# Kernel optimization log

Hardware: AMD Instinct MI355X
Metric: run time of the kernel (lower is better)

The kernel has to match this reference:

```python
import jax, jax.numpy as jnp
import numpy as np

TEMPERATURE = 0.5


def setup_inputs() -> dict:
    key = jax.random.key(0)
    k1, k2 = jax.random.split(key)
    B, D = 4096, 256
    return {
        "features": jax.random.normal(k1, (B, D), dtype=jnp.float32),
        "transformed_features": jax.random.normal(k2, (B, D), dtype=jnp.float32),
    }


def reference(features, transformed_features):
    B = features.shape[0]
    N = 2 * B
    all_features = jnp.concatenate([features, transformed_features], axis=0)  # [2B, D]
    # F.normalize(dim=-1): L2 normalize with eps clamp of 1e-12 on the norm
    norm = jnp.maximum(jnp.linalg.norm(all_features, axis=-1, keepdims=True), 1e-12)
    all_features = all_features / norm
    sim = jnp.matmul(all_features, all_features.T)  # [2B, 2B]
    # positive pairs: diag at offsets +B and -B
    pos = jnp.concatenate([jnp.diagonal(sim, offset=B), jnp.diagonal(sim, offset=-B)], axis=0)  # [2B]
    numerator = jnp.exp(pos / TEMPERATURE)
    # torch code multiplies sim by (1 - eye) BEFORE exp, so diagonal contributes exp(0)=1 to the sum
    sim_no_diag = sim * (1.0 - jnp.eye(N, dtype=sim.dtype))
    denominator = jnp.exp(sim_no_diag / TEMPERATURE).sum(axis=1)  # [2B]
    losses = -jnp.log(numerator / denominator)
    return jnp.sum(losses) / N
```

## Files before the change

### kernel.cpp

```cpp
#include <hip/hip_runtime.h>

#define B_ROWS 4096
#define N_ROWS 8192
#define DDIM   256
#define IT2    2.885390081777927f

#define BM 128
#define BN 128
#define BK 64
#define SPLITS 32
#define CT_PER_BLOCK (N_ROWS / BN / SPLITS)
#define NPARTS (SPLITS * 2)

typedef unsigned short ushort_t;
typedef __bf16 bf16x8 __attribute__((ext_vector_type(8)));
typedef float  f32x4  __attribute__((ext_vector_type(4)));

__device__ __forceinline__ ushort_t f2bf(float x) {
    union { float f; unsigned u; } a; a.f = x;
    unsigned r = a.u + 0x7fffu + ((a.u >> 16) & 1u);
    return (ushort_t)(r >> 16);
}

__device__ __forceinline__ void gload_lds16(const void* g, void* l) {
    __builtin_amdgcn_global_load_lds(
        (const __attribute__((address_space(1))) unsigned int*)g,
        (__attribute__((address_space(3))) unsigned int*)l,
        16, 0, 0);
}

__global__ __launch_bounds__(256) void k_normalize(
        const float* __restrict__ feats, const float* __restrict__ tfeats,
        ushort_t* __restrict__ Xb, float* __restrict__ norms) {
    int w = threadIdx.x >> 6, l = threadIdx.x & 63;
    int row = blockIdx.x * 4 + w;
    const float* src = (row < B_ROWS) ? feats + (size_t)row * DDIM
                                      : tfeats + (size_t)(row - B_ROWS) * DDIM;
    float4 v = ((const float4*)src)[l];
    float ss = v.x*v.x + v.y*v.y + v.z*v.z + v.w*v.w;
    #pragma unroll
    for (int m = 1; m < 64; m <<= 1) ss += __shfl_xor(ss, m);
    float nrm = fmaxf(sqrtf(ss), 1e-12f);
    float inv = 1.0f / nrm;
    ushort4 o;
    o.x = f2bf(v.x * inv); o.y = f2bf(v.y * inv);
    o.z = f2bf(v.z * inv); o.w = f2bf(v.w * inv);
    ((ushort4*)(Xb + (size_t)row * DDIM))[l] = o;
    if (l == 0) norms[row] = nrm;
}

__global__ __launch_bounds__(256) void k_pos(
        const float* __restrict__ feats, const float* __restrict__ tfeats,
        const float* __restrict__ norms, float* __restrict__ posv) {
    int w = threadIdx.x >> 6, l = threadIdx.x & 63;
    int i = blockIdx.x * 4 + w;
    float4 a = ((const float4*)(feats  + (size_t)i * DDIM))[l];
    float4 b = ((const float4*)(tfeats + (size_t)i * DDIM))[l];
    float d = a.x*b.x + a.y*b.y + a.z*b.z + a.w*b.w;
    #pragma unroll
    for (int m = 1; m < 64; m <<= 1) d += __shfl_xor(d, m);
    if (l == 0) posv[i] = d / (norms[i] * norms[i + B_ROWS]);
}

__global__ __launch_bounds__(256) void k_gemm(
        const ushort_t* __restrict__ Xb, float* __restrict__ parts) {
    __shared__ ushort_t ldsA[BM * BK];
    __shared__ ushort_t ldsB[BN * BK];

    int bid = blockIdx.x;
    int rt = bid >> 5;
    int split = bid & 31;
    int rowbase = rt * BM;
    int t = threadIdx.x;
    int l = t & 63;
    int w = t >> 6;
    int wm = w >> 1, wn = w & 1;

    float sums[4][4];
    #pragma unroll
    for (int m = 0; m < 4; m++)
        #pragma unroll
        for (int j = 0; j < 4; j++) sums[m][j] = 0.0f;

    for (int ct = 0; ct < CT_PER_BLOCK; ++ct) {
        int colbase = (split * CT_PER_BLOCK + ct) * BN;
        f32x4 acc[4][4];
        #pragma unroll
        for (int m = 0; m < 4; m++)
            #pragma unroll
            for (int n = 0; n < 4; n++) acc[m][n] = (f32x4){0.f, 0.f, 0.f, 0.f};

        for (int kb = 0; kb < DDIM; kb += BK) {
            #pragma unroll
            for (int i = 0; i < 4; i++) {
                int o   = (i * 256 + t) * 16;
                int row = o >> 7;
                int cb  = o & 127;
                int scb = cb ^ ((row & 7) << 4);
                const char* ga = (const char*)Xb +
                    ((size_t)(rowbase + row) * DDIM + kb) * 2 + scb;
                gload_lds16(ga, (char*)ldsA + o);
                const char* gb = (const char*)Xb +
                    ((size_t)(colbase + row) * DDIM + kb) * 2 + scb;
                gload_lds16(gb, (char*)ldsB + o);
            }
            __syncthreads();

            #pragma unroll
            for (int ks = 0; ks < 2; ks++) {
                bf16x8 af[4], bfr[4];
                int cbw = ((l >> 4) * 16) + ks * 64;
                #pragma unroll
                for (int m = 0; m < 4; m++) {
                    int row  = wm * 64 + m * 16 + (l & 15);
                    int addr = row * 128 + (cbw ^ ((row & 7) << 4));
                    af[m] = *(const bf16x8*)((const char*)ldsA + addr);
                }
                #pragma unroll
                for (int n = 0; n < 4; n++) {
                    int row  = wn * 64 + n * 16 + (l & 15);
                    int addr = row * 128 + (cbw ^ ((row & 7) << 4));
                    bfr[n] = *(const bf16x8*)((const char*)ldsB + addr);
                }
                #pragma unroll
                for (int m = 0; m < 4; m++)
                    #pragma unroll
                    for (int n = 0; n < 4; n++)
                        acc[m][n] = __builtin_amdgcn_mfma_f32_16x16x32_bf16(
                            af[m], bfr[n], acc[m][n], 0, 0, 0);
            }
            __syncthreads();
        }

        #pragma unroll
        for (int m = 0; m < 4; m++) {
            #pragma unroll
            for (int j = 0; j < 4; j++) {
                int grow = rowbase + wm * 64 + m * 16 + (l >> 4) * 4 + j;
                float s = 0.0f;
                #pragma unroll
                for (int n = 0; n < 4; n++) {
                    int gcol = colbase + wn * 64 + n * 16 + (l & 15);
                    float v = acc[m][n][j];
                    float e = exp2f(v * IT2);
                    s += (grow == gcol) ? 1.0f : e;
                }
                sums[m][j] += s;
            }
        }
    }

    #pragma unroll
    for (int m = 0; m < 4; m++)
        #pragma unroll
        for (int j = 0; j < 4; j++) {
            float v = sums[m][j];
            v += __shfl_xor(v, 1);
            v += __shfl_xor(v, 2);
            v += __shfl_xor(v, 4);
            v += __shfl_xor(v, 8);
            sums[m][j] = v;
        }

    if ((l & 15) == 0) {
        int part = split * 2 + wn;
        #pragma unroll
        for (int m = 0; m < 4; m++)
            #pragma unroll
            for (int j = 0; j < 4; j++) {
                int grow = rowbase + wm * 64 + m * 16 + (l >> 4) * 4 + j;
                parts[(size_t)part * N_ROWS + grow] = sums[m][j];
            }
    }
}

__global__ __launch_bounds__(256) void k_rowreduce(
        const float* __restrict__ parts, float* __restrict__ bsums) {
    int row = blockIdx.x * 256 + threadIdx.x;
    float den = 0.0f;
    #pragma unroll 8
    for (int p = 0; p < NPARTS; p++) den += parts[(size_t)p * N_ROWS + row];
    float v = logf(den);
    #pragma unroll
    for (int m = 1; m < 64; m <<= 1) v += __shfl_xor(v, m);
    __shared__ float red[4];
    if ((threadIdx.x & 63) == 0) red[threadIdx.x >> 6] = v;
    __syncthreads();
    if (threadIdx.x == 0)
        bsums[blockIdx.x] = red[0] + red[1] + red[2] + red[3];
}

__global__ __launch_bounds__(256) void k_final(
        const float* __restrict__ bsums, const float* __restrict__ posv,
        float* __restrict__ out) {
    int t = threadIdx.x;
    float ps = 0.0f;
    for (int i = t; i < B_ROWS; i += 256) ps += posv[i];
    float lg = (t < 32) ? bsums[t] : 0.0f;
    float comb = lg - 4.0f * ps;
    #pragma unroll
    for (int m = 1; m < 64; m <<= 1) comb += __shfl_xor(comb, m);
    __shared__ float red[4];
    if ((t & 63) == 0) red[t >> 6] = comb;
    __syncthreads();
    if (t == 0) out[0] = (red[0] + red[1] + red[2] + red[3]) / (float)N_ROWS;
}

extern "C" void kernel_launch(void* const* d_in, const int* in_sizes, int n_in,
                              void* d_out, int out_size, void* d_ws, size_t ws_size,
                              hipStream_t stream) {
    const float* feats  = (const float*)d_in[0];
    const float* tfeats = (const float*)d_in[1];
    float* out = (float*)d_out;
    char* ws = (char*)d_ws;

    ushort_t* Xb    = (ushort_t*)ws;
    float*    norms = (float*)(ws + 4194304);
    float*    posv  = (float*)(ws + 4227072);
    float*    parts = (float*)(ws + 4243456);
    float*    bsums = (float*)(ws + 6340608);

    k_normalize<<<N_ROWS / 4, 256, 0, stream>>>(feats, tfeats, Xb, norms);
    k_pos      <<<B_ROWS / 4, 256, 0, stream>>>(feats, tfeats, norms, posv);
    k_gemm     <<<64 * SPLITS, 256, 0, stream>>>(Xb, parts);
    k_rowreduce<<<N_ROWS / 256, 256, 0, stream>>>(parts, bsums);
    k_final    <<<1, 256, 0, stream>>>(bsums, posv, out);
}
```

Measured before the change: 119.6 us.

## Exploit symmetry of similarity matrix, compute upper-triangular tiles only, fuse norm and pos

The GEMM now covers only the upper-triangular 128x128 tile pairs (2080 blocks instead of the full grid). Each off-diagonal tile contributes both row sums and column sums of exp(sim/T), which roughly halves the MFMA and exp work. The normalize and positive-pair kernels are merged into one, dropping a launch and a second read of the inputs. In exchange there are twice as many partial buffers to reduce, a serial while-loop to decode each block's tile index, and no multi-tile loop per block to amortize setup.

```diff
diff --git a/kernel.cpp b/kernel.cpp
--- a/kernel.cpp
+++ b/kernel.cpp
@@ -6,11 +6,10 @@
 #define IT2    2.885390081777927f
 
 #define BM 128
-#define BN 128
 #define BK 64
-#define SPLITS 32
-#define CT_PER_BLOCK (N_ROWS / BN / SPLITS)
-#define NPARTS (SPLITS * 2)
+#define NTILE 64
+#define NBLK  2080
+#define NPARTS 128
 
 typedef unsigned short ushort_t;
 typedef __bf16 bf16x8 __attribute__((ext_vector_type(8)));
@@ -29,13 +28,17 @@
         16, 0, 0);
 }
 
-__global__ __launch_bounds__(256) void k_normalize(
+__global__ __launch_bounds__(256) void k_norm_pos(
         const float* __restrict__ feats, const float* __restrict__ tfeats,
-        ushort_t* __restrict__ Xb, float* __restrict__ norms) {
+        ushort_t* __restrict__ Xb, float* __restrict__ posv) {
+    __shared__ float fbuf[2][DDIM];
+    __shared__ float nsh[4];
     int w = threadIdx.x >> 6, l = threadIdx.x & 63;
-    int row = blockIdx.x * 4 + w;
-    const float* src = (row < B_ROWS) ? feats + (size_t)row * DDIM
-                                      : tfeats + (size_t)(row - B_ROWS) * DDIM;
+    int i0 = blockIdx.x * 2;
+    int pair = (w < 2) ? w : (w - 2);
+    int row  = (w < 2) ? (i0 + pair) : (i0 + pair + B_ROWS);
+    const float* src = (w < 2) ? feats + (size_t)(i0 + pair) * DDIM
+                               : tfeats + (size_t)(i0 + pair) * DDIM;
     float4 v = ((const float4*)src)[l];
     float ss = v.x*v.x + v.y*v.y + v.z*v.z + v.w*v.w;
     #pragma unroll
@@ -46,131 +49,135 @@
     o.x = f2bf(v.x * inv); o.y = f2bf(v.y * inv);
     o.z = f2bf(v.z * inv); o.w = f2bf(v.w * inv);
     ((ushort4*)(Xb + (size_t)row * DDIM))[l] = o;
-    if (l == 0) norms[row] = nrm;
-}
-
-__global__ __launch_bounds__(256) void k_pos(
-        const float* __restrict__ feats, const float* __restrict__ tfeats,
-        const float* __restrict__ norms, float* __restrict__ posv) {
-    int w = threadIdx.x >> 6, l = threadIdx.x & 63;
-    int i = blockIdx.x * 4 + w;
-    float4 a = ((const float4*)(feats  + (size_t)i * DDIM))[l];
-    float4 b = ((const float4*)(tfeats + (size_t)i * DDIM))[l];
-    float d = a.x*b.x + a.y*b.y + a.z*b.z + a.w*b.w;
-    #pragma unroll
-    for (int m = 1; m < 64; m <<= 1) d += __shfl_xor(d, m);
-    if (l == 0) posv[i] = d / (norms[i] * norms[i + B_ROWS]);
+    if (w < 2) ((float4*)fbuf[pair])[l] = v;
+    if (l == 0) nsh[w] = nrm;
+    __syncthreads();
+    if (w >= 2) {
+        float4 a = ((const float4*)fbuf[pair])[l];
+        float d = a.x*v.x + a.y*v.y + a.z*v.z + a.w*v.w;
+        #pragma unroll
+        for (int m = 1; m < 64; m <<= 1) d += __shfl_xor(d, m);
+        if (l == 0) posv[i0 + pair] = d / (nsh[pair] * nsh[w]);
+    }
 }
 
 __global__ __launch_bounds__(256) void k_gemm(
         const ushort_t* __restrict__ Xb, float* __restrict__ parts) {
     __shared__ ushort_t ldsA[BM * BK];
-    __shared__ ushort_t ldsB[BN * BK];
-
-    int bid = blockIdx.x;
-    int rt = bid >> 5;
-    int split = bid & 31;
+    __shared__ ushort_t ldsB[BM * BK];
+
+    int idx = blockIdx.x;
+    int rt = 0;
+    while (idx >= (NTILE - rt)) { idx -= (NTILE - rt); rt++; }
+    int ct = rt + idx;
+    bool isdiag = (rt == ct);
+
     int rowbase = rt * BM;
+    int colbase = ct * BM;
     int t = threadIdx.x;
     int l = t & 63;
     int w = t >> 6;
     int wm = w >> 1, wn = w & 1;
 
-    float sums[4][4];
+    f32x4 acc[4][4];
     #pragma unroll
     for (int m = 0; m < 4; m++)
         #pragma unroll
-        for (int j = 0; j < 4; j++) sums[m][j] = 0.0f;
-
-    for (int ct = 0; ct < CT_PER_BLOCK; ++ct) {
-        int colbase = (split * CT_PER_BLOCK + ct) * BN;
-        f32x4 acc[4][4];
-        #pragma unroll
-        for (int m = 0; m < 4; m++)
-            #pragma unroll
-            for (int n = 0; n < 4; n++) acc[m][n] = (f32x4){0.f, 0.f, 0.f, 0.f};
-
-        for (int kb = 0; kb < DDIM; kb += BK) {
-            #pragma unroll
-            for (int i = 0; i < 4; i++) {
-                int o   = (i * 256 + t) * 16;
-                int row = o >> 7;
-                int cb  = o & 127;
-                int scb = cb ^ ((row & 7) << 4);
-                const char* ga = (const char*)Xb +
-                    ((size_t)(rowbase + row) * DDIM + kb) * 2 + scb;
-                gload_lds16(ga, (char*)ldsA + o);
-                const char* gb = (const char*)Xb +
-                    ((size_t)(colbase + row) * DDIM + kb) * 2 + scb;
-                gload_lds16(gb, (char*)ldsB + o);
-            }
-            __syncthreads();
-
-            #pragma unroll
-            for (int ks = 0; ks < 2; ks++) {
-                bf16x8 af[4], bfr[4];
-                int cbw = ((l >> 4) * 16) + ks * 64;
+        for (int n = 0; n < 4; n++) acc[m][n] = (f32x4){0.f, 0.f, 0.f, 0.f};
+
+    for (int kb = 0; kb < DDIM; kb += BK) {
+        #pragma unroll
+        for (int i = 0; i < 4; i++) {
+            int o   = (i * 256 + t) * 16;
+            int row = o >> 7;
+            int cb  = o & 127;
+            int scb = cb ^ ((row & 7) << 4);
+            const char* ga = (const char*)Xb +
+                ((size_t)(rowbase + row) * DDIM + kb) * 2 + scb;
+            gload_lds16(ga, (char*)ldsA + o);
+            const char* gb = (const char*)Xb +
+                ((size_t)(colbase + row) * DDIM + kb) * 2 + scb;
+            gload_lds16(gb, (char*)ldsB + o);
+        }
+        __syncthreads();
+
+        #pragma unroll
+        for (int ks = 0; ks < 2; ks++) {
+            bf16x8 af[4], bfr[4];
+            int cbw = ((l >> 4) * 16) + ks * 64;
+            #pragma unroll
+            for (int m = 0; m < 4; m++) {
+                int row  = wm * 64 + m * 16 + (l & 15);
+                int addr = row * 128 + (cbw ^ ((row & 7) << 4));
+                af[m] = *(const bf16x8*)((const char*)ldsA + addr);
+            }
+            #pragma unroll
+            for (int n = 0; n < 4; n++) {
+                int row  = wn * 64 + n * 16 + (l & 15);
+                int addr = row * 128 + (cbw ^ ((row & 7) << 4));
+                bfr[n] = *(const bf16x8*)((const char*)ldsB + addr);
+            }
+            #pragma unroll
+            for (int m = 0; m < 4; m++)
                 #pragma unroll
-                for (int m = 0; m < 4; m++) {
-                    int row  = wm * 64 + m * 16 + (l & 15);
-                    int addr = row * 128 + (cbw ^ ((row & 7) << 4));
-                    af[m] = *(const bf16x8*)((const char*)ldsA + addr);
-                }
-                #pragma unroll
-                for (int n = 0; n < 4; n++) {
-                    int row  = wn * 64 + n * 16 + (l & 15);
-                    int addr = row * 128 + (cbw ^ ((row & 7) << 4));
-                    bfr[n] = *(const bf16x8*)((const char*)ldsB + addr);
-                }
-                #pragma unroll
-                for (int m = 0; m < 4; m++)
-                    #pragma unroll
-                    for (int n = 0; n < 4; n++)
-                        acc[m][n] = __builtin_amdgcn_mfma_f32_16x16x32_bf16(
-                            af[m], bfr[n], acc[m][n], 0, 0, 0);
-            }
-            __syncthreads();
-        }
-
-        #pragma unroll
-        for (int m = 0; m < 4; m++) {
-            #pragma unroll
-            for (int j = 0; j < 4; j++) {
-                int grow = rowbase + wm * 64 + m * 16 + (l >> 4) * 4 + j;
-                float s = 0.0f;
-                #pragma unroll
-                for (int n = 0; n < 4; n++) {
-                    int gcol = colbase + wn * 64 + n * 16 + (l & 15);
-                    float v = acc[m][n][j];
-                    float e = exp2f(v * IT2);
-                    s += (grow == gcol) ? 1.0f : e;
-                }
-                sums[m][j] += s;
-            }
-        }
-    }
-
+                for (int n = 0; n < 4; n++)
+                    acc[m][n] = __builtin_amdgcn_mfma_f32_16x16x32_bf16(
+                        af[m], bfr[n], acc[m][n], 0, 0, 0);
+        }
+        __syncthreads();
+    }
+
+    float rs[4][4];
+    float cs[4];
     #pragma unroll
     for (int m = 0; m < 4; m++)
         #pragma unroll
+        for (int j = 0; j < 4; j++) rs[m][j] = 0.0f;
+    #pragma unroll
+    for (int n = 0; n < 4; n++) cs[n] = 0.0f;
+
+    #pragma unroll
+    for (int m = 0; m < 4; m++) {
+        #pragma unroll
         for (int j = 0; j < 4; j++) {
-            float v = sums[m][j];
+            int grow = rowbase + wm * 64 + m * 16 + (l >> 4) * 4 + j;
+            #pragma unroll
+            for (int n = 0; n < 4; n++) {
+                int gcol = colbase + wn * 64 + n * 16 + (l & 15);
+                float e = exp2f(acc[m][n][j] * IT2);
+                if (isdiag && grow == gcol) e = 1.0f;
+                rs[m][j] += e;
+                cs[n]    += e;
+            }
+        }
+    }
+
+    #pragma unroll
+    for (int m = 0; m < 4; m++)
+        #pragma unroll
+        for (int j = 0; j < 4; j++) {
+            float v = rs[m][j];
             v += __shfl_xor(v, 1);
             v += __shfl_xor(v, 2);
             v += __shfl_xor(v, 4);
             v += __shfl_xor(v, 8);
-            sums[m][j] = v;
-        }
-
-    if ((l & 15) == 0) {
-        int part = split * 2 + wn;
-        #pragma unroll
-        for (int m = 0; m < 4; m++)
-            #pragma unroll
-            for (int j = 0; j < 4; j++) {
+            if ((l & 15) == 0) {
                 int grow = rowbase + wm * 64 + m * 16 + (l >> 4) * 4 + j;
-                parts[(size_t)part * N_ROWS + grow] = sums[m][j];
-            }
+                parts[(size_t)(ct * 2 + wn) * N_ROWS + grow] = v;
+            }
+        }
+
+    if (!isdiag) {
+        #pragma unroll
+        for (int n = 0; n < 4; n++) {
+            float v = cs[n];
+            v += __shfl_xor(v, 16);
+            v += __shfl_xor(v, 32);
+            if (l < 16) {
+                int gcol = colbase + wn * 64 + n * 16 + l;
+                parts[(size_t)(rt * 2 + wm) * N_ROWS + gcol] = v;
+            }
+        }
     }
 }
 
@@ -215,14 +222,12 @@
     char* ws = (char*)d_ws;
 
     ushort_t* Xb    = (ushort_t*)ws;
-    float*    norms = (float*)(ws + 4194304);
-    float*    posv  = (float*)(ws + 4227072);
-    float*    parts = (float*)(ws + 4243456);
-    float*    bsums = (float*)(ws + 6340608);
-
-    k_normalize<<<N_ROWS / 4, 256, 0, stream>>>(feats, tfeats, Xb, norms);
-    k_pos      <<<B_ROWS / 4, 256, 0, stream>>>(feats, tfeats, norms, posv);
-    k_gemm     <<<64 * SPLITS, 256, 0, stream>>>(Xb, parts);
+    float*    posv  = (float*)(ws + 4194304);
+    float*    parts = (float*)(ws + 4210688);
+    float*    bsums = (float*)(ws + 8404992);
+
+    k_norm_pos <<<B_ROWS / 2, 256, 0, stream>>>(feats, tfeats, Xb, posv);
+    k_gemm     <<<NBLK, 256, 0, stream>>>(Xb, parts);
     k_rowreduce<<<N_ROWS / 256, 256, 0, stream>>>(parts, bsums);
     k_final    <<<1, 256, 0, stream>>>(bsums, posv, out);
 }
```

Result: faster. 115.9 us (-3.1%).
